# Kernel optimization log

Measured on AMD Instinct MI355X. Metric: run time of the kernel, lower is better.

## Reference

```python
import jax, jax.numpy as jnp
import numpy as np

N = 100000; EI = 1600000; EC = 800000; G = 2000
FD = 512; H1 = 32; H2 = 32; EMB = 128; NH = 4
EPS = 1e-5


def setup_inputs() -> dict:
    key = jax.random.key(0)
    ks = jax.random.split(key, 30)
    p = lambda k, shp: (jax.random.normal(k, shp, jnp.float32) * 0.05)
    inp = {
        'feat': jax.random.normal(ks[0], (N, FD), jnp.float32),
        'inter_src': jax.random.randint(ks[1], (EI,), 0, N),
        'inter_dst': jax.random.randint(ks[2], (EI,), 0, N),
        'cross_src': jax.random.randint(ks[3], (EC,), 0, N),
        'cross_dst': jax.random.randint(ks[4], (EC,), 0, N),
        'graph_ids': jnp.sort(jax.random.randint(ks[5], (N,), 0, G)),
        # layer1
        'W_gc1': p(ks[6], (FD, NH * H1)), 'b_gc1': p(ks[7], (NH * H1,)),
        'W_gat1': p(ks[8], (FD, NH * H1)), 'al1': p(ks[9], (NH, H1)), 'ar1': p(ks[10], (NH, H1)), 'b_gat1': p(ks[11], (NH * H1,)),
        # layer2
        'W_gc2': p(ks[12], (NH * H1, NH * H2)), 'b_gc2': p(ks[13], (NH * H2,)),
        'W_gat2': p(ks[14], (NH * H1, NH * H2)), 'al2': p(ks[15], (NH, H2)), 'ar2': p(ks[16], (NH, H2)), 'b_gat2': p(ks[17], (NH * H2,)),
        # layer3
        'W_gc3': p(ks[18], (NH * H2, EMB)), 'b_gc3': p(ks[19], (EMB,)),
        'W_gat3': p(ks[20], (NH * H2, EMB)), 'al3': p(ks[21], (1, EMB)), 'ar3': p(ks[22], (1, EMB)), 'b_gat3': p(ks[23], (EMB,)),
        # batchnorms (gamma ones, beta zeros)
        'g1': jnp.ones((NH * H1,), jnp.float32), 'be1': jnp.zeros((NH * H1,), jnp.float32),
        'g2': jnp.ones((NH * H2,), jnp.float32), 'be2': jnp.zeros((NH * H2,), jnp.float32),
        'g3': jnp.ones((EMB,), jnp.float32), 'be3': jnp.zeros((EMB,), jnp.float32),
    }
    return inp


def _leaky(x):
    return jnp.where(x >= 0, x, 0.2 * x)


def _graph_conv(x, W, b, src, dst):
    # DGL GraphConv, norm='both': D_out^{-1/2} A D_in^{-1/2} X W + b (degrees clamped to >=1)
    ones = jnp.ones(src.shape[0], x.dtype)
    dout = jnp.clip(jax.ops.segment_sum(ones, src, num_segments=N), 1.0)
    din = jnp.clip(jax.ops.segment_sum(ones, dst, num_segments=N), 1.0)
    xw = (x @ W) * (dout ** -0.5)[:, None]          # project first (in >= out)
    agg = jax.ops.segment_sum(xw[src], dst, num_segments=N)
    return agg * (din ** -0.5)[:, None] + b


def _gat(x, W, al, ar, b, src, dst, H, d):
    # DGL GATConv: per-edge additive attention with edge softmax over incoming edges
    f = (x @ W).reshape(-1, H, d)                    # [N,H,d]
    el = jnp.sum(f * al, -1)                         # [N,H]
    er = jnp.sum(f * ar, -1)
    e = _leaky(el[src] + er[dst])                    # [E,H]
    m = jax.ops.segment_max(e, dst, num_segments=N)
    ex = jnp.exp(e - m[dst])
    s = jax.ops.segment_sum(ex, dst, num_segments=N)
    alpha = ex / s[dst]                              # [E,H]
    out = jax.ops.segment_sum(alpha[:, :, None] * f[src], dst, num_segments=N)
    return out + b.reshape(1, H, d), alpha


def _bn(x, g, b):
    mu = x.mean(0)
    v = jnp.mean((x - mu) ** 2, 0)
    return g * (x - mu) / jnp.sqrt(v + EPS) + b


def reference(feat, inter_src, inter_dst, cross_src, cross_dst, graph_ids,
              W_gc1, b_gc1, W_gat1, al1, ar1, b_gat1,
              W_gc2, b_gc2, W_gat2, al2, ar2, b_gat2,
              W_gc3, b_gc3, W_gat3, al3, ar3, b_gat3,
              g1, be1, g2, be2, g3, be3):
    h = feat
    hi = _graph_conv(h, W_gc1, b_gc1, inter_src, inter_dst)
    hc, _ = _gat(h, W_gat1, al1, ar1, b_gat1, cross_src, cross_dst, NH, H1)
    h = _bn(_leaky(hi + hc.reshape(N, -1)), g1, be1)
    hi = _graph_conv(h, W_gc2, b_gc2, inter_src, inter_dst)
    hc, _ = _gat(h, W_gat2, al2, ar2, b_gat2, cross_src, cross_dst, NH, H2)
    h = _bn(_leaky(hi + hc.reshape(N, -1)), g2, be2)
    h1 = _graph_conv(h, W_gc3, b_gc3, inter_src, inter_dst)
    h2, att = _gat(h, W_gat3, al3, ar3, b_gat3, cross_src, cross_dst, 1, EMB)
    h = _bn(h1 + h2[:, 0, :], g3, be3)
    att_sum = jax.ops.segment_sum(att[:, 0], cross_src, num_segments=N)   # [N]
    wh = h * att_sum[:, None]
    gsum = jax.ops.segment_sum(wh, graph_ids, num_segments=G)
    cnt = jnp.clip(jax.ops.segment_sum(jnp.ones(N, h.dtype), graph_ids, num_segments=G), 1.0)
    frag_embeddings = gsum / cnt[:, None]                                  # [G,EMB]
    return frag_embeddings, att_sum
```

## Files before the change

### kernel.cpp

```cpp
#include <hip/hip_runtime.h>
#include <math.h>

#define NN 100000
#define EIE 1600000
#define ECE 800000
#define GG 2000
#define FDIM 512
#define CC 128
#define BNEPS 1e-5f
#define SLOTI 48
#define SLOTC 32
#define GEMM1_BLOCKS 782
#define FILL_BLOCKS 3128
#define FUSED_BLOCKS 3910

static inline int cdiv(long a, long b){ return (int)((a+b-1)/b); }

typedef __attribute__((ext_vector_type(8))) short short8;
typedef __attribute__((ext_vector_type(4))) float f32x4;

__device__ __forceinline__ unsigned short f2bf(float f){
  unsigned u = __float_as_uint(f);
  u += 0x7fffu + ((u >> 16) & 1u);
  return (unsigned short)(u >> 16);
}
__device__ __forceinline__ float bf2f(unsigned short h){
  return __uint_as_float(((unsigned)h) << 16);
}
__device__ __forceinline__ float2 ldbf2(const unsigned short* p){
  ushort2 u = *(const ushort2*)p;
  return make_float2(bf2f(u.x), bf2f(u.y));
}

__device__ __forceinline__ size_t wt_off(int n, int k) {
  return (size_t)(k >> 5)*8192 + (((n >> 4)*4 + ((k >> 3) & 3))*16 + (n & 15))*8 + (k & 7);
}
__global__ void k_pack_all(const float* __restrict__ Wgc1, const float* __restrict__ Wgat1,
                           const float* __restrict__ Wgc2, const float* __restrict__ Wgat2,
                           const float* __restrict__ Wgc3, const float* __restrict__ Wgat3,
                           unsigned short* __restrict__ Wth1, unsigned short* __restrict__ Wtl1,
                           unsigned short* __restrict__ Wth2, unsigned short* __restrict__ Wtl2,
                           unsigned short* __restrict__ Wth3, unsigned short* __restrict__ Wtl3) {
  int t = blockIdx.x*256 + threadIdx.x;
  const float *W1, *W2; unsigned short *oh, *ol; int FIN, tt;
  if (t < 131072)      { W1=Wgc1; W2=Wgat1; oh=Wth1; ol=Wtl1; FIN=512; tt=t; }
  else if (t < 163840) { W1=Wgc2; W2=Wgat2; oh=Wth2; ol=Wtl2; FIN=128; tt=t-131072; }
  else if (t < 196608) { W1=Wgc3; W2=Wgat3; oh=Wth3; ol=Wtl3; FIN=128; tt=t-163840; }
  else return;
  int n = tt / FIN, k = tt % FIN;
  float v = (n < 128) ? W1[(size_t)k*128 + n] : W2[(size_t)k*128 + (n-128)];
  unsigned short h = f2bf(v);
  size_t o = wt_off(n, k);
  oh[o] = h;
  ol[o] = f2bf(v - bf2f(h));
}

__global__ __launch_bounds__(512)
void k_fill_gemm1(const int* __restrict__ isrc, const int* __restrict__ idst,
                  const int* __restrict__ csrc, const int* __restrict__ cdst,
                  int* __restrict__ cnt_i, int* __restrict__ eid_i,
                  int* __restrict__ cnt_c, int* __restrict__ eid_c,
                  int* __restrict__ dout, float* __restrict__ att,
                  const float* __restrict__ xf,
                  const unsigned short* __restrict__ Bh, const unsigned short* __restrict__ Bl,
                  unsigned short* __restrict__ Y1, unsigned short* __restrict__ Y2) {
  __shared__ __attribute__((aligned(16))) unsigned short sAh[4096];
  __shared__ __attribute__((aligned(16))) unsigned short sBh[8192];
  __shared__ __attribute__((aligned(16))) unsigned short sBl[8192];
  int r = blockIdx.x;
  int tid = threadIdx.x;

  if (r % 5 != 0) {
    int fi = r - 1 - (r-1)/5;
    int e = fi*512 + tid;
    if (e < EIE) {
      int d = idst[e];
      int p = atomicAdd(&cnt_i[d], 1);
      if (p < SLOTI) eid_i[d*SLOTI + p] = isrc[e];
      atomicAdd(&dout[isrc[e]], 1);
    }
    if (e < ECE) {
      int d = cdst[e];
      int p = atomicAdd(&cnt_c[d], 1);
      if (p < SLOTC) eid_c[d*SLOTC + p] = csrc[e];
    }
    if (e < NN) att[e] = 0.f;
    return;
  }

  int row0 = (r/5)*128;
  int lane = tid & 63, wid = tid >> 6;
  int wm = wid >> 2, wn = wid & 3;
  int l15 = lane & 15, quad = lane >> 4;

  f32x4 acc[4][4];
  #pragma unroll
  for (int mt = 0; mt < 4; ++mt)
    #pragma unroll
    for (int nt = 0; nt < 4; ++nt) acc[mt][nt] = (f32x4){0.f,0.f,0.f,0.f};

  for (int k0 = 0; k0 < FDIM; k0 += 32) {
    #pragma unroll
    for (int i = 0; i < 2; ++i) {
      int idx = tid + i*512;
      int rr = idx >> 3, c = idx & 7;
      int gr = row0 + rr; if (gr > NN-1) gr = NN-1;
      float4 v = *(const float4*)(xf + (size_t)gr*FDIM + k0 + c*4);
      ushort4 hh;
      hh.x = f2bf(v.x); hh.y = f2bf(v.y); hh.z = f2bf(v.z); hh.w = f2bf(v.w);
      *(ushort4*)&sAh[(((rr>>4)*4 + (c>>1))*16 + (rr&15))*8 + (c&1)*4] = hh;
    }
    const unsigned short* bhk = Bh + (size_t)k0*256;
    const unsigned short* blk = Bl + (size_t)k0*256;
    #pragma unroll
    for (int i = 0; i < 2; ++i) {
      int idx = tid + i*512;
      *(float4*)&sBh[idx*8] = *(const float4*)(bhk + idx*8);
      *(float4*)&sBl[idx*8] = *(const float4*)(blk + idx*8);
    }
    __syncthreads();
    short8 ah[4];
    #pragma unroll
    for (int mt = 0; mt < 4; ++mt)
      ah[mt] = *(const short8*)&sAh[(((wm*4+mt)*4 + quad)*16 + l15)*8];
    #pragma unroll
    for (int nt = 0; nt < 4; ++nt) {
      int off = (((wn*4+nt)*4 + quad)*16 + l15)*8;
      short8 bh = *(const short8*)&sBh[off];
      short8 bl = *(const short8*)&sBl[off];
      #pragma unroll
      for (int mt = 0; mt < 4; ++mt) {
        acc[mt][nt] = __builtin_amdgcn_mfma_f32_16x16x32_bf16(ah[mt], bh, acc[mt][nt], 0,0,0);
        acc[mt][nt] = __builtin_amdgcn_mfma_f32_16x16x32_bf16(ah[mt], bl, acc[mt][nt], 0,0,0);
      }
    }
    __syncthreads();
  }
  unsigned short* Y = (wn < 2) ? Y1 : Y2;
  int colbase = (wn & 1)*64;
  #pragma unroll
  for (int mt = 0; mt < 4; ++mt) {
    #pragma unroll
    for (int rr = 0; rr < 4; ++rr) {
      int row = row0 + (wm*4+mt)*16 + quad*4 + rr;
      if (row >= NN) continue;
      #pragma unroll
      for (int nt = 0; nt < 4; ++nt)
        Y[(size_t)row*CC + colbase + nt*16 + l15] = f2bf(acc[mt][nt][rr]);
    }
  }
}

__global__ __launch_bounds__(512)
void k_gemm2(const unsigned short* __restrict__ xb,
             const unsigned short* __restrict__ Bh, const unsigned short* __restrict__ Bl,
             const float* __restrict__ bnsc, const float* __restrict__ bnsh,
             unsigned short* __restrict__ Y1, unsigned short* __restrict__ Y2) {
  __shared__ __attribute__((aligned(16))) unsigned short sAh[4096];
  __shared__ __attribute__((aligned(16))) unsigned short sBh[8192];
  __shared__ __attribute__((aligned(16))) unsigned short sBl[8192];
  int tid = threadIdx.x;
  int row0 = blockIdx.x*128;
  int lane = tid & 63, wid = tid >> 6;
  int wm = wid >> 2, wn = wid & 3;
  int l15 = lane & 15, quad = lane >> 4;

  f32x4 acc[4][4];
  #pragma unroll
  for (int mt = 0; mt < 4; ++mt)
    #pragma unroll
    for (int nt = 0; nt < 4; ++nt) acc[mt][nt] = (f32x4){0.f,0.f,0.f,0.f};

  for (int k0 = 0; k0 < CC; k0 += 32) {
    int rr = tid >> 2, c16 = tid & 3;
    int gr = row0 + rr; if (gr > NN-1) gr = NN-1;
    short8 u = *(const short8*)(xb + (size_t)gr*CC + k0 + c16*8);
    short8 o;
    #pragma unroll
    for (int j = 0; j < 8; ++j) {
      float f = bf2f((unsigned short)u[j]);
      f = f*bnsc[k0 + c16*8 + j] + bnsh[k0 + c16*8 + j];
      o[j] = (short)f2bf(f);
    }
    *(short8*)&sAh[(((rr>>4)*4 + c16)*16 + (rr&15))*8] = o;

    const unsigned short* bhk = Bh + (size_t)k0*256;
    const unsigned short* blk = Bl + (size_t)k0*256;
    #pragma unroll
    for (int i = 0; i < 2; ++i) {
      int idx = tid + i*512;
      *(float4*)&sBh[idx*8] = *(const float4*)(bhk + idx*8);
      *(float4*)&sBl[idx*8] = *(const float4*)(blk + idx*8);
    }
    __syncthreads();
    short8 ah[4];
    #pragma unroll
    for (int mt = 0; mt < 4; ++mt)
      ah[mt] = *(const short8*)&sAh[(((wm*4+mt)*4 + quad)*16 + l15)*8];
    #pragma unroll
    for (int nt = 0; nt < 4; ++nt) {
      int off = (((wn*4+nt)*4 + quad)*16 + l15)*8;
      short8 bh = *(const short8*)&sBh[off];
      short8 bl = *(const short8*)&sBl[off];
      #pragma unroll
      for (int mt = 0; mt < 4; ++mt) {
        acc[mt][nt] = __builtin_amdgcn_mfma_f32_16x16x32_bf16(ah[mt], bh, acc[mt][nt], 0,0,0);
        acc[mt][nt] = __builtin_amdgcn_mfma_f32_16x16x32_bf16(ah[mt], bl, acc[mt][nt], 0,0,0);
      }
    }
    __syncthreads();
  }
  unsigned short* Y = (wn < 2) ? Y1 : Y2;
  int colbase = (wn & 1)*64;
  #pragma unroll
  for (int mt = 0; mt < 4; ++mt) {
    #pragma unroll
    for (int rr = 0; rr < 4; ++rr) {
      int row = row0 + (wm*4+mt)*16 + quad*4 + rr;
      if (row >= NN) continue;
      #pragma unroll
      for (int nt = 0; nt < 4; ++nt)
        Y[(size_t)row*CC + colbase + nt*16 + l15] = f2bf(acc[mt][nt][rr]);
    }
  }
}

template<int H>
__global__ __launch_bounds__(256)
void k_elr2(const unsigned short* __restrict__ f, const float* __restrict__ al,
            const float* __restrict__ ar, float* __restrict__ el, float* __restrict__ er,
            float* __restrict__ csq) {
  if (blockIdx.x == 0) csq[threadIdx.x] = 0.f;
  int lane = threadIdx.x & 63;
  int n = blockIdx.x*4 + (threadIdx.x >> 6);
  if (n >= NN) return;
  int c2 = lane*2;
  float2 v = ldbf2(f + (size_t)n*CC + c2);
  float2 a = *(const float2*)(al + c2);
  float2 b = *(const float2*)(ar + c2);
  float pa = v.x*a.x + v.y*a.y;
  float pb = v.x*b.x + v.y*b.y;
  const int W = (H == 1) ? 64 : 16;
  #pragma unroll
  for (int m = W>>1; m >= 1; m >>= 1) { pa += __shfl_xor(pa, m); pb += __shfl_xor(pb, m); }
  if ((lane & (W-1)) == 0) {
    int h = lane / W;
    el[(size_t)n*H + h] = pa;
    er[(size_t)n*H + h] = pb;
  }
}

template<int H, bool ATT, bool LEAKY>
__global__ __launch_bounds__(256)
void k_gather_fused(const unsigned short* __restrict__ A1, const unsigned short* __restrict__ A2,
                    const int* __restrict__ cnt_i, const int* __restrict__ eid_i,
                    const int* __restrict__ cnt_c, const int* __restrict__ eid_c,
                    const int* __restrict__ dout,
                    const float* __restrict__ el, const float* __restrict__ er,
                    const float* __restrict__ bgc, const float* __restrict__ bgat,
                    unsigned short* __restrict__ out, float* __restrict__ att) {
  int lane = threadIdx.x & 63;
  int row = blockIdx.x*4 + (threadIdx.x >> 6);
  if (row >= NN) return;
  int grp = lane >> 4;
  int l4  = lane & 15;
  int c8  = l4*8;

  int deg = cnt_i[row];
  int lo = row*SLOTI, hi = lo + min(deg, SLOTI);
  float ax[8];
  #pragma unroll
  for (int k = 0; k < 8; ++k) ax[k] = 0.f;
  int j = lo + grp;
  for (; j + 4 < hi; j += 8) {
    int s0 = eid_i[j], s1 = eid_i[j+4];
    float d0 = rsqrtf((float)max(dout[s0], 1));
    float d1 = rsqrtf((float)max(dout[s1], 1));
    short8 u0 = *(const short8*)(A1 + (size_t)s0*CC + c8);
    short8 u1 = *(const short8*)(A1 + (size_t)s1*CC + c8);
    #pragma unroll
    for (int k = 0; k < 8; ++k)
      ax[k] += d0*bf2f((unsigned short)u0[k]) + d1*bf2f((unsigned short)u1[k]);
  }
  if (j < hi) {
    int s0 = eid_i[j];
    float d0 = rsqrtf((float)max(dout[s0], 1));
    short8 u0 = *(const short8*)(A1 + (size_t)s0*CC + c8);
    #pragma unroll
    for (int k = 0; k < 8; ++k) ax[k] += d0*bf2f((unsigned short)u0[k]);
  }
  float sc = rsqrtf((float)max(deg, 1));

  int h = (H == 1) ? 0 : (l4 >> 2);
  float erd = er[(size_t)row*H + h];
  int degc = cnt_c[row];
  int lo2 = row*SLOTC, hi2 = lo2 + min(degc, SLOTC);
  float gacc[8];
  #pragma unroll
  for (int k = 0; k < 8; ++k) gacc[k] = 0.f;
  float denom = 0.f;
  for (j = lo2 + grp; j < hi2; j += 4) {
    int s = eid_c[j];
    float v = el[(size_t)s*H + h] + erd;
    v = (v >= 0.f) ? v : 0.2f*v;
    float w = __expf(v);
    denom += w;
    short8 u = *(const short8*)(A2 + (size_t)s*CC + c8);
    #pragma unroll
    for (int k = 0; k < 8; ++k) gacc[k] += w * bf2f((unsigned short)u[k]);
  }

  #pragma unroll
  for (int m = 16; m <= 32; m <<= 1) {
    denom += __shfl_xor(denom, m);
    #pragma unroll
    for (int k = 0; k < 8; ++k) {
      ax[k]   += __shfl_xor(ax[k], m);
      gacc[k] += __shfl_xor(gacc[k], m);
    }
  }
  float inv = (denom > 0.f) ? 1.0f/denom : 0.f;

  if (ATT) {
    for (j = lo2 + grp; j < hi2; j += 4) {
      int s = eid_c[j];
      if (l4 == 0) {
        float v = el[(size_t)s*H] + erd;
        v = (v >= 0.f) ? v : 0.2f*v;
        atomicAdd(&att[s], __expf(v)*inv);
      }
    }
  }

  if (grp == 0) {
    float4 b1a = *(const float4*)(bgc + c8);
    float4 b1b = *(const float4*)(bgc + c8 + 4);
    float4 b2a = *(const float4*)(bgat + c8);
    float4 b2b = *(const float4*)(bgat + c8 + 4);
    float bb1[8] = {b1a.x,b1a.y,b1a.z,b1a.w,b1b.x,b1b.y,b1b.z,b1b.w};
    float bb2[8] = {b2a.x,b2a.y,b2a.z,b2a.w,b2b.x,b2b.y,b2b.z,b2b.w};
    short8 ov;
    #pragma unroll
    for (int k = 0; k < 8; ++k) {
      float o = ax[k]*sc + bb1[k] + gacc[k]*inv + bb2[k];
      if (LEAKY) o = (o >= 0.f) ? o : 0.2f*o;
      ov[k] = (short)f2bf(o);
    }
    *(short8*)(out + (size_t)row*CC + c8) = ov;
  }
}

__global__ __launch_bounds__(256)
void k_bn_stats(const unsigned short* __restrict__ t, float* __restrict__ csq) {
  __shared__ float red[4][128];
  int lane = threadIdx.x & 63, g = threadIdx.x >> 6;
  int c2 = lane*2;
  float s0=0.f, s1=0.f, q0=0.f, q1=0.f;
  for (int r = blockIdx.x*4 + g; r < NN; r += gridDim.x*4) {
    float2 v = ldbf2(t + (size_t)r*CC + c2);
    s0 += v.x; s1 += v.y; q0 += v.x*v.x; q1 += v.y*v.y;
  }
  red[g][c2] = s0; red[g][c2+1] = s1;
  __syncthreads();
  if (threadIdx.x < 128) {
    float a = red[0][threadIdx.x] + red[1][threadIdx.x] + red[2][threadIdx.x] + red[3][threadIdx.x];
    atomicAdd(&csq[threadIdx.x], a);
  }
  __syncthreads();
  red[g][c2] = q0; red[g][c2+1] = q1;
  __syncthreads();
  if (threadIdx.x < 128) {
    float a = red[0][threadIdx.x] + red[1][threadIdx.x] + red[2][threadIdx.x] + red[3][threadIdx.x];
    atomicAdd(&csq[128 + threadIdx.x], a);
  }
}

__global__ void k_bn_coef(const float* __restrict__ csq,
                          const float* __restrict__ g, const float* __restrict__ be,
                          float* __restrict__ sc, float* __restrict__ sh) {
  int c = threadIdx.x;
  float mu = csq[c] * (1.f/NN);
  float var = csq[128+c] * (1.f/NN) - mu*mu;
  float r = rsqrtf(var + BNEPS);
  float s = g[c]*r;
  sc[c] = s;
  sh[c] = be[c] - s*mu;
}

__global__ void k_pool_bn(const unsigned short* __restrict__ t, const float* __restrict__ att,
                          const int* __restrict__ gids, const float* __restrict__ bnsc,
                          const float* __restrict__ bnsh, float* __restrict__ frag) {
  int g = blockIdx.x;
  __shared__ int se[2];
  if (threadIdx.x < 2) {
    int target = g + threadIdx.x;
    int lo = 0, hi = NN;
    while (lo < hi) { int mid = (lo + hi) >> 1; if (gids[mid] < target) lo = mid + 1; else hi = mid; }
    se[threadIdx.x] = lo;
  }
  __syncthreads();
  int lo = se[0], hi = se[1];
  int col = threadIdx.x;
  float scv = bnsc[col], shv = bnsh[col];
  float acc = 0.f;
  for (int n = lo; n < hi; ++n) acc += (bf2f(t[(size_t)n*CC + col])*scv + shv) * att[n];
  frag[(size_t)g*CC + col] = acc / (float)max(hi - lo, 1);
}

extern "C" void kernel_launch(void* const* d_in, const int* in_sizes, int n_in,
                              void* d_out, int out_size, void* d_ws, size_t ws_size,
                              hipStream_t stream) {
  const float* feat  = (const float*)d_in[0];
  const int* isrc    = (const int*)d_in[1];
  const int* idst    = (const int*)d_in[2];
  const int* csrc    = (const int*)d_in[3];
  const int* cdst    = (const int*)d_in[4];
  const int* gids    = (const int*)d_in[5];
  const float* W_gc1 = (const float*)d_in[6];  const float* b_gc1 = (const float*)d_in[7];
  const float* W_gat1= (const float*)d_in[8];  const float* al1   = (const float*)d_in[9];
  const float* ar1   = (const float*)d_in[10]; const float* b_gat1= (const float*)d_in[11];
  const float* W_gc2 = (const float*)d_in[12]; const float* b_gc2 = (const float*)d_in[13];
  const float* W_gat2= (const float*)d_in[14]; const float* al2   = (const float*)d_in[15];
  const float* ar2   = (const float*)d_in[16]; const float* b_gat2= (const float*)d_in[17];
  const float* W_gc3 = (const float*)d_in[18]; const float* b_gc3 = (const float*)d_in[19];
  const float* W_gat3= (const float*)d_in[20]; const float* al3   = (const float*)d_in[21];
  const float* ar3   = (const float*)d_in[22]; const float* b_gat3= (const float*)d_in[23];
  const float* g1 = (const float*)d_in[24]; const float* be1 = (const float*)d_in[25];
  const float* g2 = (const float*)d_in[26]; const float* be2 = (const float*)d_in[27];
  const float* g3 = (const float*)d_in[28]; const float* be3 = (const float*)d_in[29];

  const size_t NC = (size_t)NN*CC;
  float* el   = (float*)d_ws;
  float* er   = el + (size_t)NN*4;
  float* csq  = er + (size_t)NN*4;
  float* bnsc = csq + 256;
  float* bnsh = bnsc + CC;
  unsigned short* B  = (unsigned short*)(bnsh + CC);
  unsigned short* A1 = B + NC;
  unsigned short* A2 = A1 + NC;
  unsigned short* Wth1 = A2 + NC;
  unsigned short* Wtl1 = Wth1 + 256*FDIM;
  unsigned short* Wth2 = Wtl1 + 256*FDIM;
  unsigned short* Wtl2 = Wth2 + 256*CC;
  unsigned short* Wth3 = Wtl2 + 256*CC;
  unsigned short* Wtl3 = Wth3 + 256*CC;
  int* cnt_i  = (int*)(Wtl3 + 256*CC);
  int* cnt_c  = cnt_i + NN;
  int* dout   = cnt_c + NN;
  int* eid_i  = dout + NN;
  int* eid_c  = eid_i + (size_t)NN*SLOTI;

  float* frag = (float*)d_out;
  float* att  = frag + (size_t)GG*CC;

  hipMemsetAsync(cnt_i, 0, 3*(size_t)NN*sizeof(int), stream);
  k_pack_all<<<cdiv(196608,256), 256, 0, stream>>>(W_gc1, W_gat1, W_gc2, W_gat2, W_gc3, W_gat3,
                                                   Wth1, Wtl1, Wth2, Wtl2, Wth3, Wtl3);
  k_fill_gemm1<<<FUSED_BLOCKS, 512, 0, stream>>>(isrc, idst, csrc, cdst,
                                                 cnt_i, eid_i, cnt_c, eid_c, dout, att,
                                                 feat, Wth1, Wtl1, A1, A2);

  k_elr2<4><<<cdiv(NN,4), 256, 0, stream>>>(A2, al1, ar1, el, er, csq);
  k_gather_fused<4,false,true><<<cdiv(NN,4), 256, 0, stream>>>(A1, A2, cnt_i, eid_i,
                                                               cnt_c, eid_c, dout, el, er,
                                                               b_gc1, b_gat1, B, nullptr);
  k_bn_stats<<<256, 256, 0, stream>>>(B, csq);
  k_bn_coef<<<1, 128, 0, stream>>>(csq, g1, be1, bnsc, bnsh);

  k_gemm2<<<cdiv(NN,128), 512, 0, stream>>>(B, Wth2, Wtl2, bnsc, bnsh, A1, A2);
  k_elr2<4><<<cdiv(NN,4), 256, 0, stream>>>(A2, al2, ar2, el, er, csq);
  k_gather_fused<4,false,true><<<cdiv(NN,4), 256, 0, stream>>>(A1, A2, cnt_i, eid_i,
                                                               cnt_c, eid_c, dout, el, er,
                                                               b_gc2, b_gat2, B, nullptr);
  k_bn_stats<<<256, 256, 0, stream>>>(B, csq);
  k_bn_coef<<<1, 128, 0, stream>>>(csq, g2, be2, bnsc, bnsh);

  k_gemm2<<<cdiv(NN,128), 512, 0, stream>>>(B, Wth3, Wtl3, bnsc, bnsh, A1, A2);
  k_elr2<1><<<cdiv(NN,4), 256, 0, stream>>>(A2, al3, ar3, el, er, csq);
  k_gather_fused<1,true,false><<<cdiv(NN,4), 256, 0, stream>>>(A1, A2, cnt_i, eid_i,
                                                               cnt_c, eid_c, dout, el, er,
                                                               b_gc3, b_gat3, B, att);
  k_bn_stats<<<256, 256, 0, stream>>>(B, csq);
  k_bn_coef<<<1, 128, 0, stream>>>(csq, g3, be3, bnsc, bnsh);

  k_pool_bn<<<GG, 128, 0, stream>>>(B, att, gids, bnsc, bnsh, frag);
}
```

Measured before the change: 1.037 ms.

## Fuse GAT attention logits into GEMM epilogues and unroll gather loops deeper

```diff
diff --git a/kernel.cpp b/kernel.cpp
--- a/kernel.cpp
+++ b/kernel.cpp
@@ -10,8 +10,6 @@
 #define BNEPS 1e-5f
 #define SLOTI 48
 #define SLOTC 32
-#define GEMM1_BLOCKS 782
-#define FILL_BLOCKS 3128
 #define FUSED_BLOCKS 3910
 
 static inline int cdiv(long a, long b){ return (int)((a+b-1)/b); }
@@ -55,6 +53,7 @@
   ol[o] = f2bf(v - bf2f(h));
 }
 
+
 __global__ __launch_bounds__(512)
 void k_fill_gemm1(const int* __restrict__ isrc, const int* __restrict__ idst,
                   const int* __restrict__ csrc, const int* __restrict__ cdst,
@@ -63,6 +62,8 @@
                   int* __restrict__ dout, float* __restrict__ att,
                   const float* __restrict__ xf,
                   const unsigned short* __restrict__ Bh, const unsigned short* __restrict__ Bl,
+                  const float* __restrict__ al, const float* __restrict__ ar,
+                  float* __restrict__ el, float* __restrict__ er,
                   unsigned short* __restrict__ Y1, unsigned short* __restrict__ Y2) {
   __shared__ __attribute__((aligned(16))) unsigned short sAh[4096];
   __shared__ __attribute__((aligned(16))) unsigned short sBh[8192];
@@ -149,12 +150,44 @@
         Y[(size_t)row*CC + colbase + nt*16 + l15] = f2bf(acc[mt][nt][rr]);
     }
   }
-}
-
+  if (wn >= 2) {
+    float alv[4], arv[4];
+    #pragma unroll
+    for (int nt = 0; nt < 4; ++nt) {
+      int col = colbase + nt*16 + l15;
+      alv[nt] = al[col]; arv[nt] = ar[col];
+    }
+    int hb = (wn & 1)*2;
+    #pragma unroll
+    for (int mt = 0; mt < 4; ++mt) {
+      #pragma unroll
+      for (int rr = 0; rr < 4; ++rr) {
+        float pa0 = acc[mt][0][rr]*alv[0] + acc[mt][1][rr]*alv[1];
+        float pb0 = acc[mt][0][rr]*arv[0] + acc[mt][1][rr]*arv[1];
+        float pa1 = acc[mt][2][rr]*alv[2] + acc[mt][3][rr]*alv[3];
+        float pb1 = acc[mt][2][rr]*arv[2] + acc[mt][3][rr]*arv[3];
+        #pragma unroll
+        for (int m = 1; m <= 8; m <<= 1) {
+          pa0 += __shfl_xor(pa0, m); pb0 += __shfl_xor(pb0, m);
+          pa1 += __shfl_xor(pa1, m); pb1 += __shfl_xor(pb1, m);
+        }
+        int row = row0 + (wm*4+mt)*16 + quad*4 + rr;
+        if (l15 == 0 && row < NN) {
+          el[(size_t)row*4 + hb]   = pa0;  er[(size_t)row*4 + hb]   = pb0;
+          el[(size_t)row*4 + hb+1] = pa1;  er[(size_t)row*4 + hb+1] = pb1;
+        }
+      }
+    }
+  }
+}
+
+template<bool ELR>
 __global__ __launch_bounds__(512)
 void k_gemm2(const unsigned short* __restrict__ xb,
              const unsigned short* __restrict__ Bh, const unsigned short* __restrict__ Bl,
              const float* __restrict__ bnsc, const float* __restrict__ bnsh,
+             const float* __restrict__ al, const float* __restrict__ ar,
+             float* __restrict__ el, float* __restrict__ er,
              unsigned short* __restrict__ Y1, unsigned short* __restrict__ Y2) {
   __shared__ __attribute__((aligned(16))) unsigned short sAh[4096];
   __shared__ __attribute__((aligned(16))) unsigned short sBh[8192];
@@ -221,6 +254,35 @@
       #pragma unroll
       for (int nt = 0; nt < 4; ++nt)
         Y[(size_t)row*CC + colbase + nt*16 + l15] = f2bf(acc[mt][nt][rr]);
+    }
+  }
+  if (ELR && wn >= 2) {
+    float alv[4], arv[4];
+    #pragma unroll
+    for (int nt = 0; nt < 4; ++nt) {
+      int col = colbase + nt*16 + l15;
+      alv[nt] = al[col]; arv[nt] = ar[col];
+    }
+    int hb = (wn & 1)*2;
+    #pragma unroll
+    for (int mt = 0; mt < 4; ++mt) {
+      #pragma unroll
+      for (int rr = 0; rr < 4; ++rr) {
+        float pa0 = acc[mt][0][rr]*alv[0] + acc[mt][1][rr]*alv[1];
+        float pb0 = acc[mt][0][rr]*arv[0] + acc[mt][1][rr]*arv[1];
+        float pa1 = acc[mt][2][rr]*alv[2] + acc[mt][3][rr]*alv[3];
+        float pb1 = acc[mt][2][rr]*arv[2] + acc[mt][3][rr]*arv[3];
+        #pragma unroll
+        for (int m = 1; m <= 8; m <<= 1) {
+          pa0 += __shfl_xor(pa0, m); pb0 += __shfl_xor(pb0, m);
+          pa1 += __shfl_xor(pa1, m); pb1 += __shfl_xor(pb1, m);
+        }
+        int row = row0 + (wm*4+mt)*16 + quad*4 + rr;
+        if (l15 == 0 && row < NN) {
+          el[(size_t)row*4 + hb]   = pa0;  er[(size_t)row*4 + hb]   = pb0;
+          el[(size_t)row*4 + hb+1] = pa1;  er[(size_t)row*4 + hb+1] = pb1;
+        }
+      }
     }
   }
 }
@@ -272,6 +334,21 @@
   #pragma unroll
   for (int k = 0; k < 8; ++k) ax[k] = 0.f;
   int j = lo + grp;
+  for (; j + 12 < hi; j += 16) {
+    int s0 = eid_i[j], s1 = eid_i[j+4], s2 = eid_i[j+8], s3 = eid_i[j+12];
+    float d0 = rsqrtf((float)max(dout[s0], 1));
+    float d1 = rsqrtf((float)max(dout[s1], 1));
+    float d2 = rsqrtf((float)max(dout[s2], 1));
+    float d3 = rsqrtf((float)max(dout[s3], 1));
+    short8 u0 = *(const short8*)(A1 + (size_t)s0*CC + c8);
+    short8 u1 = *(const short8*)(A1 + (size_t)s1*CC + c8);
+    short8 u2 = *(const short8*)(A1 + (size_t)s2*CC + c8);
+    short8 u3 = *(const short8*)(A1 + (size_t)s3*CC + c8);
+    #pragma unroll
+    for (int k = 0; k < 8; ++k)
+      ax[k] += d0*bf2f((unsigned short)u0[k]) + d1*bf2f((unsigned short)u1[k])
+             + d2*bf2f((unsigned short)u2[k]) + d3*bf2f((unsigned short)u3[k]);
+  }
   for (; j + 4 < hi; j += 8) {
     int s0 = eid_i[j], s1 = eid_i[j+4];
     float d0 = rsqrtf((float)max(dout[s0], 1));
@@ -299,7 +376,22 @@
   #pragma unroll
   for (int k = 0; k < 8; ++k) gacc[k] = 0.f;
   float denom = 0.f;
-  for (j = lo2 + grp; j < hi2; j += 4) {
+  j = lo2 + grp;
+  for (; j + 4 < hi2; j += 8) {
+    int s0 = eid_c[j], s1 = eid_c[j+4];
+    float v0 = el[(size_t)s0*H + h] + erd;
+    float v1 = el[(size_t)s1*H + h] + erd;
+    v0 = (v0 >= 0.f) ? v0 : 0.2f*v0;
+    v1 = (v1 >= 0.f) ? v1 : 0.2f*v1;
+    float w0 = __expf(v0), w1 = __expf(v1);
+    denom += w0 + w1;
+    short8 u0 = *(const short8*)(A2 + (size_t)s0*CC + c8);
+    short8 u1 = *(const short8*)(A2 + (size_t)s1*CC + c8);
+    #pragma unroll
+    for (int k = 0; k < 8; ++k)
+      gacc[k] += w0*bf2f((unsigned short)u0[k]) + w1*bf2f((unsigned short)u1[k]);
+  }
+  if (j < hi2) {
     int s = eid_c[j];
     float v = el[(size_t)s*H + h] + erd;
     v = (v >= 0.f) ? v : 0.2f*v;
@@ -375,16 +467,18 @@
   }
 }
 
-__global__ void k_bn_coef(const float* __restrict__ csq,
+__global__ void k_bn_coef(const float* __restrict__ csqc, float* __restrict__ csq,
                           const float* __restrict__ g, const float* __restrict__ be,
                           float* __restrict__ sc, float* __restrict__ sh) {
   int c = threadIdx.x;
-  float mu = csq[c] * (1.f/NN);
-  float var = csq[128+c] * (1.f/NN) - mu*mu;
+  float sv = csqc[c], qv = csqc[128+c];
+  float mu = sv * (1.f/NN);
+  float var = qv * (1.f/NN) - mu*mu;
   float r = rsqrtf(var + BNEPS);
   float s = g[c]*r;
   sc[c] = s;
   sh[c] = be[c] - s*mu;
+  csq[c] = 0.f; csq[128+c] = 0.f;
 }
 
 __global__ void k_pool_bn(const unsigned short* __restrict__ t, const float* __restrict__ att,
@@ -454,34 +548,35 @@
   float* att  = frag + (size_t)GG*CC;
 
   hipMemsetAsync(cnt_i, 0, 3*(size_t)NN*sizeof(int), stream);
+  hipMemsetAsync(csq, 0, 256*sizeof(float), stream);
   k_pack_all<<<cdiv(196608,256), 256, 0, stream>>>(W_gc1, W_gat1, W_gc2, W_gat2, W_gc3, W_gat3,
                                                    Wth1, Wtl1, Wth2, Wtl2, Wth3, Wtl3);
   k_fill_gemm1<<<FUSED_BLOCKS, 512, 0, stream>>>(isrc, idst, csrc, cdst,
                                                  cnt_i, eid_i, cnt_c, eid_c, dout, att,
-                                                 feat, Wth1, Wtl1, A1, A2);
-
-  k_elr2<4><<<cdiv(NN,4), 256, 0, stream>>>(A2, al1, ar1, el, er, csq);
+                                                 feat, Wth1, Wtl1, al1, ar1, el, er, A1, A2);
+
   k_gather_fused<4,false,true><<<cdiv(NN,4), 256, 0, stream>>>(A1, A2, cnt_i, eid_i,
                                                                cnt_c, eid_c, dout, el, er,
                                                                b_gc1, b_gat1, B, nullptr);
   k_bn_stats<<<256, 256, 0, stream>>>(B, csq);
-  k_bn_coef<<<1, 128, 0, stream>>>(csq, g1, be1, bnsc, bnsh);
-
-  k_gemm2<<<cdiv(NN,128), 512, 0, stream>>>(B, Wth2, Wtl2, bnsc, bnsh, A1, A2);
-  k_elr2<4><<<cdiv(NN,4), 256, 0, stream>>>(A2, al2, ar2, el, er, csq);
+  k_bn_coef<<<1, 128, 0, stream>>>(csq, csq, g1, be1, bnsc, bnsh);
+
+  k_gemm2<true><<<cdiv(NN,128), 512, 0, stream>>>(B, Wth2, Wtl2, bnsc, bnsh,
+                                                  al2, ar2, el, er, A1, A2);
   k_gather_fused<4,false,true><<<cdiv(NN,4), 256, 0, stream>>>(A1, A2, cnt_i, eid_i,
                                                                cnt_c, eid_c, dout, el, er,
                                                                b_gc2, b_gat2, B, nullptr);
   k_bn_stats<<<256, 256, 0, stream>>>(B, csq);
-  k_bn_coef<<<1, 128, 0, stream>>>(csq, g2, be2, bnsc, bnsh);
-
-  k_gemm2<<<cdiv(NN,128), 512, 0, stream>>>(B, Wth3, Wtl3, bnsc, bnsh, A1, A2);
+  k_bn_coef<<<1, 128, 0, stream>>>(csq, csq, g2, be2, bnsc, bnsh);
+
+  k_gemm2<false><<<cdiv(NN,128), 512, 0, stream>>>(B, Wth3, Wtl3, bnsc, bnsh,
+                                                   nullptr, nullptr, nullptr, nullptr, A1, A2);
   k_elr2<1><<<cdiv(NN,4), 256, 0, stream>>>(A2, al3, ar3, el, er, csq);
   k_gather_fused<1,true,false><<<cdiv(NN,4), 256, 0, stream>>>(A1, A2, cnt_i, eid_i,
                                                                cnt_c, eid_c, dout, el, er,
                                                                b_gc3, b_gat3, B, att);
   k_bn_stats<<<256, 256, 0, stream>>>(B, csq);
-  k_bn_coef<<<1, 128, 0, stream>>>(csq, g3, be3, bnsc, bnsh);
+  k_bn_coef<<<1, 128, 0, stream>>>(csq, csq, g3, be3, bnsc, bnsh);
 
   k_pool_bn<<<GG, 128, 0, stream>>>(B, att, gids, bnsc, bnsh, frag);
 }
```

After: 1.040 ms. Within noise of the previous version (+0.4%).
